# Kernel optimization log

Hardware: AMD Instinct MI355X
Metric: run time of the kernel (lower is better)

The kernel has to match this reference:

```python
import jax, jax.numpy as jnp
import numpy as np
from jax import lax

B, CIN, COUT, K, N = 128, 32, 64, 3, 56
TAU, BETA = 0.5, 4.0


def _build_templates(n, tau, beta):
    # dist[mu_i, mu_j, i, j] = |i-mu_i| + |j-mu_j|
    r = np.arange(n)
    dist = np.abs(r[:, None, None, None] - r[None, None, :, None]) + \
           np.abs(r[None, :, None, None] - r[None, None, None, :])
    tpos = tau * np.maximum(1.0 - beta * dist / n, -1.0)          # [n,n,n,n]
    tpos = tpos.reshape(n * n, n, n).astype(np.float32)
    tneg = np.full((1, n, n), -tau, dtype=np.float32)
    return np.concatenate([tpos, tneg], axis=0)                   # [n*n+1, n, n]


def setup_inputs() -> dict:
    key = jax.random.key(0)
    k1, k2, k3 = jax.random.split(key, 3)
    x = jax.random.normal(k1, (B, CIN, N, N), dtype=jnp.float32)
    W = jax.random.normal(k2, (COUT, CIN, K, K), dtype=jnp.float32) * 0.05
    b = jax.random.normal(k3, (COUT,), dtype=jnp.float32) * 0.05
    templates = jnp.asarray(_build_templates(N, TAU, BETA))
    return {"x": x, "W": W, "b": b, "templates": templates}


def reference(x, W, b, templates):
    # conv2d padding=1, stride 1 + ReLU
    y = lax.conv_general_dilated(
        x, W, window_strides=(1, 1), padding=[(1, 1), (1, 1)],
        dimension_numbers=("NCHW", "OIHW", "NCHW"))
    y = jax.nn.relu(y + b[None, :, None, None])                   # [B,C,H,W]
    Bc, C, H, Wd = y.shape
    # per-(batch,channel) argmax over flattened spatial map -> template index
    idx = jnp.argmax(y.reshape(Bc, C, H * Wd), axis=-1)           # [B,C] int
    masks = templates[idx]                                        # [B,C,H,W]
    masked = y * masks
    return masked * (masked > 0)
```

## Files before the change

### kernel.cpp

```cpp
#include <hip/hip_runtime.h>
#include <cstddef>

#define NSP   56
#define NPX   3136
#define CINN  32
#define COUTN 64
#define NB    128
#define CO_PB 8
#define ROWS  7
#define NSTRIP 8
#define THR   448
#define SROWS 9
#define XCOL  68

__global__ __launch_bounds__(256)
void wtrans(const float* __restrict__ W, float* __restrict__ w2)
{
    int idx = blockIdx.x * 256 + threadIdx.x;
    if (idx < COUTN * CINN * 9) {
        int co_l = idx & 7;
        int t    = idx >> 3;
        int c    = t & 31;
        t >>= 5;
        int kk   = t % 9;
        int cog  = t / 9;
        w2[idx] = W[(size_t)(cog * 8 + co_l) * (CINN * 9) + c * 9 + kk];
    }
}

__global__ __launch_bounds__(THR, 4)
void conv_emul_pass1(const float* __restrict__ x,
                     const float* __restrict__ w2,
                     const float* __restrict__ bias,
                     float* __restrict__ y,
                     int* __restrict__ amax)
{
    __shared__ float xs[SROWS][CINN][XCOL];
    __shared__ float rv[7][CO_PB];
    __shared__ int   ri[7][CO_PB];

    const int tid = threadIdx.x;
    const int ty  = tid >> 6;
    const int tx  = tid & 63;
    const int b       = blockIdx.x >> 3;
    const int cog     = blockIdx.x & 7;
    const int co_base = cog * CO_PB;

    const float* xb = x  + (size_t)b * CINN * NPX;
    const float* wq = w2 + (size_t)cog * (9 * CINN * CO_PB);

    const int sc = tid / 14;
    const int sv = tid - sc * 14;
    const float* xg = xb + (size_t)sc * NPX + 4 * sv;

    for (int t = tid; t < SROWS * CINN * 2; t += THR) {
        int rr  = t / (CINN * 2);
        int rem = t - rr * (CINN * 2);
        int c   = rem >> 1;
        xs[rr][c][(rem & 1) ? 60 : 3] = 0.f;
    }

    float v1[CO_PB]; int i1[CO_PB];
    #pragma unroll
    for (int co = 0; co < CO_PB; ++co) { v1[co] = -1.f; i1[co] = 0; }

    float* yo = y + (size_t)(b * COUTN + co_base) * NPX;

    #pragma unroll 1
    for (int g = 0; g < NSTRIP; ++g) {
        if (g) __syncthreads();

        #pragma unroll
        for (int rr = 0; rr < SROWS; ++rr) {
            int gr = 7 * g + rr - 1;
            float4 val = make_float4(0.f, 0.f, 0.f, 0.f);
            if ((unsigned)gr < (unsigned)NSP)
                val = *(const float4*)(xg + gr * NSP);
            *(float4*)&xs[rr][sc][4 + 4 * sv] = val;
        }
        __syncthreads();

        float acc[CO_PB];
        #pragma unroll
        for (int co = 0; co < CO_PB; ++co) acc[co] = 0.f;

        if (tx < NSP) {
            #pragma unroll
            for (int kh = 0; kh < 3; ++kh) {
                #pragma unroll
                for (int kw = 0; kw < 3; ++kw) {
                    float xv[CINN];
                    #pragma unroll
                    for (int c = 0; c < CINN; ++c)
                        xv[c] = xs[ty + kh][c][tx + kw + 3];
                    const float* wk = wq + (kh * 3 + kw) * (CINN * CO_PB);
                    #pragma unroll
                    for (int c = 0; c < CINN; ++c) {
                        #pragma unroll
                        for (int co = 0; co < CO_PB; ++co)
                            acc[co] = fmaf(xv[c], wk[c * CO_PB + co], acc[co]);
                    }
                }
            }
            int p = (7 * g + ty) * NSP + tx;
            #pragma unroll
            for (int co = 0; co < CO_PB; ++co) {
                float v = acc[co] + bias[co_base + co];
                v = fmaxf(v, 0.f);
                yo[(size_t)co * NPX + p] = v;
                if (v > v1[co]) { v1[co] = v; i1[co] = p; }
            }
        }
    }

    #pragma unroll
    for (int co = 0; co < CO_PB; ++co) {
        float bv = v1[co]; int bi = i1[co];
        #pragma unroll
        for (int off = 32; off > 0; off >>= 1) {
            float ov = __shfl_xor(bv, off);
            int   oi = __shfl_xor(bi, off);
            if (ov > bv || (ov == bv && oi < bi)) { bv = ov; bi = oi; }
        }
        if ((tid & 63) == 0) { rv[ty][co] = bv; ri[ty][co] = bi; }
    }
    __syncthreads();
    if (tid < CO_PB) {
        float bv = rv[0][tid]; int bi = ri[0][tid];
        #pragma unroll
        for (int w = 1; w < 7; ++w) {
            float ov = rv[w][tid]; int oi = ri[w][tid];
            if (ov > bv || (ov == bv && oi < bi)) { bv = ov; bi = oi; }
        }
        amax[b * COUTN + co_base + tid] = bi;
    }
}

__global__ __launch_bounds__(256)
void mask_apply_pass2(float* __restrict__ y,
                      const float* __restrict__ tmpl,
                      const int* __restrict__ amax)
{
    const int bc = blockIdx.x;
    const int idx = amax[bc];
    const float4* tp = (const float4*)(tmpl + (size_t)idx * NPX);
    float4* yp = (float4*)(y + (size_t)bc * NPX);
    #pragma unroll 1
    for (int p = threadIdx.x; p < NPX / 4; p += 256) {
        float4 a = yp[p];
        float4 t = tp[p];
        a.x *= t.x; a.y *= t.y; a.z *= t.z; a.w *= t.w;
        a.x = a.x > 0.f ? a.x : 0.f;
        a.y = a.y > 0.f ? a.y : 0.f;
        a.z = a.z > 0.f ? a.z : 0.f;
        a.w = a.w > 0.f ? a.w : 0.f;
        yp[p] = a;
    }
}

extern "C" void kernel_launch(void* const* d_in, const int* in_sizes, int n_in,
                              void* d_out, int out_size, void* d_ws, size_t ws_size,
                              hipStream_t stream)
{
    (void)in_sizes; (void)n_in; (void)ws_size; (void)out_size;
    const float* x  = (const float*)d_in[0];
    const float* W  = (const float*)d_in[1];
    const float* bi = (const float*)d_in[2];
    const float* tm = (const float*)d_in[3];
    float* out = (float*)d_out;
    int*   amax = (int*)d_ws;
    float* w2   = (float*)((char*)d_ws + 32768);

    hipLaunchKernelGGL(wtrans, dim3(72), dim3(256), 0, stream, W, w2);

    dim3 grid1(NB * (COUTN / CO_PB));
    hipLaunchKernelGGL(conv_emul_pass1, grid1, dim3(THR), 0, stream,
                       x, w2, bi, out, amax);

    dim3 grid2(NB * COUTN);
    hipLaunchKernelGGL(mask_apply_pass2, grid2, dim3(256), 0, stream,
                       out, tm, amax);
}
```

Measured before the change: 415.8 us.

## Software-pipeline LDS tap loads, remap block order, hoist bias loads

Reworks the 3x3 tap loop into a triple-buffered software pipeline, so LDS reads for the next taps are issued while FMAs for the current tap run, hiding LDS latency. It also remaps block indices so that consecutive blocks share the same output-channel group across 32 batches, which may improve weight cache locality. Bias values are loaded into registers once instead of on every strip. The extra buffers raise register pressure (96 floats of staged inputs), which could cause spills or lower occupancy under the 448x4 launch bound.

```diff
diff --git a/kernel.cpp b/kernel.cpp
--- a/kernel.cpp
+++ b/kernel.cpp
@@ -42,8 +42,9 @@
     const int tid = threadIdx.x;
     const int ty  = tid >> 6;
     const int tx  = tid & 63;
-    const int b       = blockIdx.x >> 3;
-    const int cog     = blockIdx.x & 7;
+    const int i   = blockIdx.x;
+    const int cog = (i >> 5) & 7;
+    const int b   = (i & 31) | ((i >> 8) << 5);
     const int co_base = cog * CO_PB;
 
     const float* xb = x  + (size_t)b * CINN * NPX;
@@ -59,6 +60,10 @@
         int c   = rem >> 1;
         xs[rr][c][(rem & 1) ? 60 : 3] = 0.f;
     }
+
+    float bs[CO_PB];
+    #pragma unroll
+    for (int co = 0; co < CO_PB; ++co) bs[co] = bias[co_base + co];
 
     float v1[CO_PB]; int i1[CO_PB];
     #pragma unroll
@@ -85,27 +90,39 @@
         for (int co = 0; co < CO_PB; ++co) acc[co] = 0.f;
 
         if (tx < NSP) {
-            #pragma unroll
-            for (int kh = 0; kh < 3; ++kh) {
-                #pragma unroll
-                for (int kw = 0; kw < 3; ++kw) {
-                    float xv[CINN];
-                    #pragma unroll
-                    for (int c = 0; c < CINN; ++c)
-                        xv[c] = xs[ty + kh][c][tx + kw + 3];
-                    const float* wk = wq + (kh * 3 + kw) * (CINN * CO_PB);
-                    #pragma unroll
-                    for (int c = 0; c < CINN; ++c) {
-                        #pragma unroll
-                        for (int co = 0; co < CO_PB; ++co)
-                            acc[co] = fmaf(xv[c], wk[c * CO_PB + co], acc[co]);
-                    }
-                }
-            }
+            float xv0[CINN], xv1[CINN], xv2[CINN];
+
+#define LOADG(buf, gg) { \
+            const int kh_ = (gg) / 3, kw_ = (gg) % 3; \
+            _Pragma("unroll") \
+            for (int c = 0; c < CINN; ++c) \
+                buf[c] = xs[ty + kh_][c][tx + kw_ + 3]; }
+
+#define FMAG(buf, gg) { \
+            const float* wk_ = wq + (gg) * (CINN * CO_PB); \
+            _Pragma("unroll") \
+            for (int c = 0; c < CINN; ++c) { \
+                _Pragma("unroll") \
+                for (int co = 0; co < CO_PB; ++co) \
+                    acc[co] = fmaf(buf[c], wk_[c * CO_PB + co], acc[co]); } }
+
+            LOADG(xv0, 0); LOADG(xv1, 1);
+            LOADG(xv2, 2); FMAG(xv0, 0);
+            LOADG(xv0, 3); FMAG(xv1, 1);
+            LOADG(xv1, 4); FMAG(xv2, 2);
+            LOADG(xv2, 5); FMAG(xv0, 3);
+            LOADG(xv0, 6); FMAG(xv1, 4);
+            LOADG(xv1, 7); FMAG(xv2, 5);
+            LOADG(xv2, 8); FMAG(xv0, 6);
+            FMAG(xv1, 7);
+            FMAG(xv2, 8);
+#undef LOADG
+#undef FMAG
+
             int p = (7 * g + ty) * NSP + tx;
             #pragma unroll
             for (int co = 0; co < CO_PB; ++co) {
-                float v = acc[co] + bias[co_base + co];
+                float v = acc[co] + bs[co];
                 v = fmaxf(v, 0.f);
                 yo[(size_t)co * NPX + p] = v;
                 if (v > v1[co]) { v1[co] = v; i1[co] = p; }
```

Result: slower. 424.7 us (+2.1%).
